# Kernel tuning notes

Measured on AMD Instinct MI355X. Metric: run time of the kernel, lower is better.

The kernel has to match this reference:

```python
import jax, jax.numpy as jnp
import numpy as np

B, L, D, Q, H = 16, 2048, 1024, 1024, 256
NEG_NUM = -10000.0


def setup_inputs() -> dict:
    key = jax.random.key(0)
    ks = jax.random.split(key, 8)
    ctx = jax.random.normal(ks[0], (B, L, D), dtype=jnp.float32)
    query = jax.random.normal(ks[1], (B, Q), dtype=jnp.float32)
    mask = jax.random.randint(ks[2], (B, L), 0, 2, dtype=jnp.int32)
    # lin_in2proj: Linear(D+Q, H)
    lim1 = 1.0 / np.sqrt(D + Q)
    W1 = jax.random.uniform(ks[3], (H, D + Q), jnp.float32, -lim1, lim1)
    b1 = jax.random.uniform(ks[4], (H,), jnp.float32, -lim1, lim1)
    # lin_proj2score: weight_norm(Linear(H, 1)), dim=0 -> g scalar per row
    lim2 = 1.0 / np.sqrt(H)
    v = jax.random.uniform(ks[5], (1, H), jnp.float32, -lim2, lim2)
    g = jnp.linalg.norm(v).reshape(1, 1)  # weight_norm init: g = ||v||
    b2 = jax.random.uniform(ks[6], (1,), jnp.float32, -lim2, lim2)
    return {"ctx": ctx, "query": query, "mask": mask,
            "W1": W1, "b1": b1, "v": v, "g": g, "b2": b2}


def reference(ctx, query, mask, W1, b1, v, g, b2):
    d = ctx.shape[-1]
    # concat([ctx, query_expanded]) @ W1^T == ctx @ W1c^T + query @ W1q^T
    Wc, Wq = W1[:, :d], W1[:, d:]
    hid = jnp.tanh(jnp.einsum('bld,hd->blh', ctx, Wc)
                   + jnp.einsum('bq,hq->bh', query, Wq)[:, None, :]
                   + b1)                                 # (B, L, H)
    w2 = (g * v / jnp.linalg.norm(v))[0]                 # weight-normed row (H,)
    score = jnp.einsum('blh,h->bl', hid, w2) + b2[0]     # (B, L)
    score = jnp.where(mask == 1, NEG_NUM, score)
    p_ctx = jax.nn.softmax(score, axis=-1)               # (B, L)
    expected_ctx = jnp.einsum('bl,bld->bd', p_ctx, ctx)  # (B, D)
    return expected_ctx, p_ctx
```

## Files before the change

kernel.cpp:

```cpp
#include <hip/hip_runtime.h>
#include <hip/hip_bf16.h>

#define BB 16
#define LCTX 2048
#define DDIM 1024
#define QDIM 1024
#define HDIM 256
#define NEGV -10000.0f

typedef __attribute__((ext_vector_type(8))) short short8;
typedef __attribute__((ext_vector_type(4))) float f32x4;

__device__ inline unsigned short f2bf(float x) {
    unsigned int u = __float_as_uint(x);
    unsigned int r = (u + 0x7fffu + ((u >> 16) & 1u)) >> 16;
    return (unsigned short)r;
}

__global__ __launch_bounds__(256) void k_qproj(const float* __restrict__ query,
                                               const float* __restrict__ W1,
                                               const float* __restrict__ b1,
                                               float* __restrict__ qproj) {
    int bid = blockIdx.x;
    int b = bid >> 6;
    int hq = bid & 63;
    int wid = threadIdx.x >> 6, lane = threadIdx.x & 63;
    int h = hq * 4 + wid;
    const float* q = query + b * QDIM;
    const float* w = W1 + (size_t)h * (DDIM + QDIM) + DDIM;
    float s = 0.f;
    #pragma unroll 4
    for (int k = lane; k < QDIM; k += 64) s += q[k] * w[k];
    #pragma unroll
    for (int o = 32; o; o >>= 1) s += __shfl_down(s, o);
    if (lane == 0) qproj[b * HDIM + h] = s + b1[h];
}

__global__ __launch_bounds__(256) void k_prepw(const float* __restrict__ W1,
                                               const float* __restrict__ v,
                                               const float* __restrict__ g,
                                               unsigned short* __restrict__ Wc_sw,
                                               float* __restrict__ w2) {
    int bid = blockIdx.x;
    if (bid < HDIM) {
        int h = bid;
        const float* src = W1 + (size_t)h * (DDIM + QDIM);
        int hx = h & 7;
        for (int d = threadIdx.x; d < DDIM; d += 256) {
            int kt = d >> 6;
            int s  = (d >> 3) & 7;
            int dl = d & 7;
            int dp = (kt << 6) + ((s ^ hx) << 3) + dl;
            Wc_sw[h * DDIM + dp] = f2bf(src[d]);
        }
    } else {
        __shared__ float red[256];
        float vv = (threadIdx.x < HDIM) ? v[threadIdx.x] : 0.f;
        red[threadIdx.x] = vv * vv;
        __syncthreads();
        for (int o = 128; o; o >>= 1) {
            if (threadIdx.x < o) red[threadIdx.x] += red[threadIdx.x + o];
            __syncthreads();
        }
        float nrm = sqrtf(red[0]);
        if (threadIdx.x < HDIM) w2[threadIdx.x] = g[0] * vv / nrm;
    }
}

__global__ __launch_bounds__(256, 3) void k_score(const float* __restrict__ ctx,
                                                  const unsigned short* __restrict__ Wc_sw,
                                                  const float* __restrict__ qproj,
                                                  const float* __restrict__ w2,
                                                  const float* __restrict__ b2,
                                                  const int* __restrict__ mask,
                                                  float* __restrict__ score_out) {
    __shared__ unsigned short At[64 * 64];
    __shared__ unsigned short Wt[256 * 64];
    int tid = threadIdx.x;
    int wid = tid >> 6, lane = tid & 63;
    int hl = lane & 15, lhi = lane >> 4;
    int bid = blockIdx.x;
    int row0 = bid * 64;
    int b = row0 >> 11;

    float qp[4], wv[4];
    #pragma unroll
    for (int ht = 0; ht < 4; ht++) {
        int h = wid * 64 + ht * 16 + hl;
        qp[ht] = qproj[b * HDIM + h];
        wv[ht] = w2[h];
    }

    f32x4 acc[4][4];
    #pragma unroll
    for (int mt = 0; mt < 4; mt++)
        #pragma unroll
        for (int ht = 0; ht < 4; ht++)
            acc[mt][ht] = (f32x4){0.f, 0.f, 0.f, 0.f};

    int srow = tid >> 2;
    int scol = (tid & 3) * 16;
    const float* csrc = ctx + (size_t)(row0 + srow) * DDIM + scol;
    int c0 = (tid & 3) * 2;
    int sx = srow & 7;

    for (int kt = 0; kt < 16; kt++) {
        #pragma unroll
        for (int i = 0; i < 8; i++) {
            int n = i * 256 + tid;
            const unsigned short* gsrc = Wc_sw + (size_t)(n >> 3) * DDIM + kt * 64 + (n & 7) * 8;
            __builtin_amdgcn_global_load_lds(
                (const __attribute__((address_space(1))) unsigned int*)gsrc,
                (__attribute__((address_space(3))) unsigned int*)(Wt + (i * 256 + (tid & ~63)) * 8),
                16, 0, 0);
        }
        const float* cp = csrc + kt * 64;
        float4 cv0 = *(const float4*)(cp + 0);
        float4 cv1 = *(const float4*)(cp + 4);
        float4 cv2 = *(const float4*)(cp + 8);
        float4 cv3 = *(const float4*)(cp + 12);
        short8 p0 = { (short)f2bf(cv0.x), (short)f2bf(cv0.y), (short)f2bf(cv0.z), (short)f2bf(cv0.w),
                      (short)f2bf(cv1.x), (short)f2bf(cv1.y), (short)f2bf(cv1.z), (short)f2bf(cv1.w) };
        short8 p1 = { (short)f2bf(cv2.x), (short)f2bf(cv2.y), (short)f2bf(cv2.z), (short)f2bf(cv2.w),
                      (short)f2bf(cv3.x), (short)f2bf(cv3.y), (short)f2bf(cv3.z), (short)f2bf(cv3.w) };
        *(short8*)(At + srow * 64 + (((c0 + 0) ^ sx) << 3)) = p0;
        *(short8*)(At + srow * 64 + (((c0 + 1) ^ sx) << 3)) = p1;
        __syncthreads();

        #pragma unroll
        for (int ks = 0; ks < 2; ks++) {
            int s = ks * 4 + lhi;
            short8 af[4], bfr[4];
            #pragma unroll
            for (int mt = 0; mt < 4; mt++) {
                int m = mt * 16 + hl;
                af[mt] = *(const short8*)(At + m * 64 + ((s ^ (m & 7)) << 3));
            }
            #pragma unroll
            for (int ht = 0; ht < 4; ht++) {
                int h = wid * 64 + ht * 16 + hl;
                bfr[ht] = *(const short8*)(Wt + h * 64 + ((s ^ (h & 7)) << 3));
            }
            #pragma unroll
            for (int mt = 0; mt < 4; mt++)
                #pragma unroll
                for (int ht = 0; ht < 4; ht++)
                    acc[mt][ht] = __builtin_amdgcn_mfma_f32_16x16x32_bf16(af[mt], bfr[ht], acc[mt][ht], 0, 0, 0);
        }
        __syncthreads();
    }

    float* sb = (float*)At;
    #pragma unroll
    for (int mt = 0; mt < 4; mt++) {
        #pragma unroll
        for (int r = 0; r < 4; r++) {
            float partial = 0.f;
            #pragma unroll
            for (int ht = 0; ht < 4; ht++) {
                float x = acc[mt][ht][r] + qp[ht];
                x = fminf(fmaxf(x, -15.f), 15.f);
                float e = __expf(2.f * x);
                partial += (e - 1.f) / (e + 1.f) * wv[ht];
            }
            #pragma unroll
            for (int o = 1; o < 16; o <<= 1) partial += __shfl_xor(partial, o);
            if (hl == 0) sb[wid * 64 + mt * 16 + lhi * 4 + r] = partial;
        }
    }
    __syncthreads();
    if (tid < 64) {
        float s = sb[tid] + sb[64 + tid] + sb[128 + tid] + sb[192 + tid] + b2[0];
        int grow = row0 + tid;
        int bb = grow >> 11, ll = grow & 2047;
        if (mask[bb * 2048 + ll] == 1) s = NEGV;
        score_out[grow] = s;
    }
}

__global__ __launch_bounds__(256) void k_softmax(float* __restrict__ p) {
    int b = blockIdx.x;
    float* row = p + b * LCTX;
    __shared__ float red[256];
    float vals[8];
    float mx = -1e30f;
    #pragma unroll
    for (int i = 0; i < 8; i++) { vals[i] = row[threadIdx.x + i * 256]; mx = fmaxf(mx, vals[i]); }
    red[threadIdx.x] = mx;
    __syncthreads();
    for (int o = 128; o; o >>= 1) {
        if (threadIdx.x < o) red[threadIdx.x] = fmaxf(red[threadIdx.x], red[threadIdx.x + o]);
        __syncthreads();
    }
    mx = red[0];
    __syncthreads();
    float sum = 0.f;
    #pragma unroll
    for (int i = 0; i < 8; i++) { vals[i] = __expf(vals[i] - mx); sum += vals[i]; }
    red[threadIdx.x] = sum;
    __syncthreads();
    for (int o = 128; o; o >>= 1) {
        if (threadIdx.x < o) red[threadIdx.x] += red[threadIdx.x + o];
        __syncthreads();
    }
    float inv = 1.f / red[0];
    #pragma unroll
    for (int i = 0; i < 8; i++) row[threadIdx.x + i * 256] = vals[i] * inv;
}

__global__ __launch_bounds__(256) void k_expected(const float* __restrict__ ctx,
                                                  const float* __restrict__ p,
                                                  float* __restrict__ part) {
    int b = blockIdx.x, dc = blockIdx.y, ls = blockIdx.z;
    int t = threadIdx.x;
    int dd = (t & 31) * 4;
    int lp = t >> 5;
    const float* base = ctx + (size_t)b * LCTX * DDIM + dc * 128 + dd;
    const float* pr = p + b * LCTX + ls * 256;
    float4 a = {0.f, 0.f, 0.f, 0.f};
    #pragma unroll 4
    for (int k = 0; k < 32; k++) {
        int l = lp + k * 8;
        float w = pr[l];
        float4 c = *(const float4*)(base + (size_t)(ls * 256 + l) * DDIM);
        a.x += w * c.x; a.y += w * c.y; a.z += w * c.z; a.w += w * c.w;
    }
    __shared__ float red[8][128];
    red[lp][dd + 0] = a.x; red[lp][dd + 1] = a.y; red[lp][dd + 2] = a.z; red[lp][dd + 3] = a.w;
    __syncthreads();
    if (t < 128) {
        float s = 0.f;
        #pragma unroll
        for (int i = 0; i < 8; i++) s += red[i][t];
        part[((size_t)ls * 16 + b) * DDIM + dc * 128 + t] = s;
    }
}

__global__ __launch_bounds__(256) void k_finish(const float* __restrict__ part,
                                                float* __restrict__ out) {
    int idx = blockIdx.x * 256 + threadIdx.x;
    float s = 0.f;
    #pragma unroll
    for (int i = 0; i < 8; i++) s += part[i * 16384 + idx];
    out[idx] = s;
}

extern "C" void kernel_launch(void* const* d_in, const int* in_sizes, int n_in,
                              void* d_out, int out_size, void* d_ws, size_t ws_size,
                              hipStream_t stream) {
    const float* ctx   = (const float*)d_in[0];
    const float* query = (const float*)d_in[1];
    const int*   mask  = (const int*)d_in[2];
    const float* W1    = (const float*)d_in[3];
    const float* b1    = (const float*)d_in[4];
    const float* v     = (const float*)d_in[5];
    const float* g     = (const float*)d_in[6];
    const float* b2    = (const float*)d_in[7];
    float* out_exp = (float*)d_out;
    float* out_p   = (float*)d_out + 16384;

    char* ws = (char*)d_ws;
    unsigned short* Wc_sw = (unsigned short*)ws;
    float* qproj = (float*)(ws + 524288);
    float* w2    = (float*)(ws + 540672);
    float* part  = (float*)(ws + 541696);

    k_qproj  <<<dim3(1024),    256, 0, stream>>>(query, W1, b1, qproj);
    k_prepw  <<<dim3(257),     256, 0, stream>>>(W1, v, g, Wc_sw, w2);
    k_score  <<<dim3(512),     256, 0, stream>>>(ctx, Wc_sw, qproj, w2, b2, mask, out_p);
    k_softmax<<<dim3(16),      256, 0, stream>>>(out_p);
    k_expected<<<dim3(16, 8, 8), 256, 0, stream>>>(ctx, out_p, part);
    k_finish <<<dim3(64),      256, 0, stream>>>(part, out_exp);
}
```

Before: 70.48 us.

## Fuse softmax and weighted context sum into score kernel without max subtraction

Merges the qproj and weight-prep kernels into one launch. The score kernel now computes unnormalized exp(score) per row and immediately accumulates exp-weighted ctx rows from the tile it just loaded, writing per-block partial sums. A small normalization kernel sums the partials and divides by the total. This drops the separate softmax, expected and finish kernels and a second pass over ctx. The max subtraction is dropped, which relies on scores being small enough that exp does not overflow, and masked rows become exactly zero instead of exp(-10000 - max).

```diff
diff --git a/kernel.cpp b/kernel.cpp
--- a/kernel.cpp
+++ b/kernel.cpp
@@ -17,33 +17,30 @@
     return (unsigned short)r;
 }
 
-__global__ __launch_bounds__(256) void k_qproj(const float* __restrict__ query,
-                                               const float* __restrict__ W1,
-                                               const float* __restrict__ b1,
-                                               float* __restrict__ qproj) {
+__global__ __launch_bounds__(256) void k_prep(const float* __restrict__ query,
+                                              const float* __restrict__ W1,
+                                              const float* __restrict__ b1,
+                                              const float* __restrict__ v,
+                                              const float* __restrict__ g,
+                                              float* __restrict__ qproj,
+                                              unsigned short* __restrict__ Wc_sw,
+                                              float* __restrict__ w2) {
     int bid = blockIdx.x;
-    int b = bid >> 6;
-    int hq = bid & 63;
-    int wid = threadIdx.x >> 6, lane = threadIdx.x & 63;
-    int h = hq * 4 + wid;
-    const float* q = query + b * QDIM;
-    const float* w = W1 + (size_t)h * (DDIM + QDIM) + DDIM;
-    float s = 0.f;
-    #pragma unroll 4
-    for (int k = lane; k < QDIM; k += 64) s += q[k] * w[k];
-    #pragma unroll
-    for (int o = 32; o; o >>= 1) s += __shfl_down(s, o);
-    if (lane == 0) qproj[b * HDIM + h] = s + b1[h];
-}
-
-__global__ __launch_bounds__(256) void k_prepw(const float* __restrict__ W1,
-                                               const float* __restrict__ v,
-                                               const float* __restrict__ g,
-                                               unsigned short* __restrict__ Wc_sw,
-                                               float* __restrict__ w2) {
-    int bid = blockIdx.x;
-    if (bid < HDIM) {
-        int h = bid;
+    if (bid < 1024) {
+        int b = bid >> 6;
+        int hq = bid & 63;
+        int wid = threadIdx.x >> 6, lane = threadIdx.x & 63;
+        int h = hq * 4 + wid;
+        const float* q = query + b * QDIM;
+        const float* w = W1 + (size_t)h * (DDIM + QDIM) + DDIM;
+        float s = 0.f;
+        #pragma unroll 4
+        for (int k = lane; k < QDIM; k += 64) s += q[k] * w[k];
+        #pragma unroll
+        for (int o = 32; o; o >>= 1) s += __shfl_down(s, o);
+        if (lane == 0) qproj[b * HDIM + h] = s + b1[h];
+    } else if (bid < 1280) {
+        int h = bid - 1024;
         const float* src = W1 + (size_t)h * (DDIM + QDIM);
         int hx = h & 7;
         for (int d = threadIdx.x; d < DDIM; d += 256) {
@@ -73,7 +70,9 @@
                                                   const float* __restrict__ w2,
                                                   const float* __restrict__ b2,
                                                   const int* __restrict__ mask,
-                                                  float* __restrict__ score_out) {
+                                                  float* __restrict__ e_ws,
+                                                  float* __restrict__ esum_ws,
+                                                  float* __restrict__ part) {
     __shared__ unsigned short At[64 * 64];
     __shared__ unsigned short Wt[256 * 64];
     int tid = threadIdx.x;
@@ -150,7 +149,8 @@
         __syncthreads();
     }
 
-    float* sb = (float*)At;
+    float* sb  = (float*)At;
+    float* sbe = sb + 256;
     #pragma unroll
     for (int mt = 0; mt < 4; mt++) {
         #pragma unroll
@@ -169,80 +169,55 @@
         }
     }
     __syncthreads();
+
     if (tid < 64) {
         float s = sb[tid] + sb[64 + tid] + sb[128 + tid] + sb[192 + tid] + b2[0];
         int grow = row0 + tid;
         int bb = grow >> 11, ll = grow & 2047;
-        if (mask[bb * 2048 + ll] == 1) s = NEGV;
-        score_out[grow] = s;
-    }
-}
-
-__global__ __launch_bounds__(256) void k_softmax(float* __restrict__ p) {
-    int b = blockIdx.x;
-    float* row = p + b * LCTX;
-    __shared__ float red[256];
-    float vals[8];
-    float mx = -1e30f;
-    #pragma unroll
-    for (int i = 0; i < 8; i++) { vals[i] = row[threadIdx.x + i * 256]; mx = fmaxf(mx, vals[i]); }
-    red[threadIdx.x] = mx;
+        float e = (mask[bb * 2048 + ll] == 1) ? 0.f : __expf(s);
+        e_ws[grow] = e;
+        sbe[tid] = e;
+        float tot = e;
+        #pragma unroll
+        for (int o = 32; o; o >>= 1) tot += __shfl_down(tot, o);
+        if (tid == 0) esum_ws[bid] = tot;
+    }
     __syncthreads();
-    for (int o = 128; o; o >>= 1) {
-        if (threadIdx.x < o) red[threadIdx.x] = fmaxf(red[threadIdx.x], red[threadIdx.x + o]);
-        __syncthreads();
-    }
-    mx = red[0];
-    __syncthreads();
-    float sum = 0.f;
-    #pragma unroll
-    for (int i = 0; i < 8; i++) { vals[i] = __expf(vals[i] - mx); sum += vals[i]; }
-    red[threadIdx.x] = sum;
-    __syncthreads();
-    for (int o = 128; o; o >>= 1) {
-        if (threadIdx.x < o) red[threadIdx.x] += red[threadIdx.x + o];
-        __syncthreads();
-    }
-    float inv = 1.f / red[0];
-    #pragma unroll
-    for (int i = 0; i < 8; i++) row[threadIdx.x + i * 256] = vals[i] * inv;
-}
-
-__global__ __launch_bounds__(256) void k_expected(const float* __restrict__ ctx,
-                                                  const float* __restrict__ p,
-                                                  float* __restrict__ part) {
-    int b = blockIdx.x, dc = blockIdx.y, ls = blockIdx.z;
-    int t = threadIdx.x;
-    int dd = (t & 31) * 4;
-    int lp = t >> 5;
-    const float* base = ctx + (size_t)b * LCTX * DDIM + dc * 128 + dd;
-    const float* pr = p + b * LCTX + ls * 256;
-    float4 a = {0.f, 0.f, 0.f, 0.f};
-    #pragma unroll 4
-    for (int k = 0; k < 32; k++) {
-        int l = lp + k * 8;
-        float w = pr[l];
-        float4 c = *(const float4*)(base + (size_t)(ls * 256 + l) * DDIM);
-        a.x += w * c.x; a.y += w * c.y; a.z += w * c.z; a.w += w * c.w;
-    }
-    __shared__ float red[8][128];
-    red[lp][dd + 0] = a.x; red[lp][dd + 1] = a.y; red[lp][dd + 2] = a.z; red[lp][dd + 3] = a.w;
-    __syncthreads();
-    if (t < 128) {
+
+    {
+        int d0 = tid * 4;
+        const float* cb = ctx + (size_t)row0 * DDIM + d0;
+        float4 a = {0.f, 0.f, 0.f, 0.f};
+        #pragma unroll 8
+        for (int l = 0; l < 64; l++) {
+            float el = sbe[l];
+            float4 c = *(const float4*)(cb + (size_t)l * DDIM);
+            a.x += el * c.x; a.y += el * c.y; a.z += el * c.z; a.w += el * c.w;
+        }
+        *(float4*)(part + (size_t)bid * DDIM + d0) = a;
+    }
+}
+
+__global__ __launch_bounds__(256) void k_norm(const float* __restrict__ e_ws,
+                                              const float* __restrict__ esum_ws,
+                                              const float* __restrict__ part,
+                                              float* __restrict__ out_exp,
+                                              float* __restrict__ out_p) {
+    int b = blockIdx.x, dc = blockIdx.y;
+    int tid = threadIdx.x;
+    float se = 0.f;
+    #pragma unroll
+    for (int j = 0; j < 32; j++) se += esum_ws[b * 32 + j];
+    float inv = 1.f / se;
+    if (tid < 128) {
+        int d = dc * 128 + tid;
         float s = 0.f;
         #pragma unroll
-        for (int i = 0; i < 8; i++) s += red[i][t];
-        part[((size_t)ls * 16 + b) * DDIM + dc * 128 + t] = s;
-    }
-}
-
-__global__ __launch_bounds__(256) void k_finish(const float* __restrict__ part,
-                                                float* __restrict__ out) {
-    int idx = blockIdx.x * 256 + threadIdx.x;
-    float s = 0.f;
-    #pragma unroll
-    for (int i = 0; i < 8; i++) s += part[i * 16384 + idx];
-    out[idx] = s;
+        for (int j = 0; j < 32; j++) s += part[(size_t)(b * 32 + j) * DDIM + d];
+        out_exp[b * DDIM + d] = s * inv;
+    }
+    int l = dc * 256 + tid;
+    out_p[b * LCTX + l] = e_ws[b * LCTX + l] * inv;
 }
 
 extern "C" void kernel_launch(void* const* d_in, const int* in_sizes, int n_in,
@@ -263,12 +238,11 @@
     unsigned short* Wc_sw = (unsigned short*)ws;
     float* qproj = (float*)(ws + 524288);
     float* w2    = (float*)(ws + 540672);
-    float* part  = (float*)(ws + 541696);
-
-    k_qproj  <<<dim3(1024),    256, 0, stream>>>(query, W1, b1, qproj);
-    k_prepw  <<<dim3(257),     256, 0, stream>>>(W1, v, g, Wc_sw, w2);
-    k_score  <<<dim3(512),     256, 0, stream>>>(ctx, Wc_sw, qproj, w2, b2, mask, out_p);
-    k_softmax<<<dim3(16),      256, 0, stream>>>(out_p);
-    k_expected<<<dim3(16, 8, 8), 256, 0, stream>>>(ctx, out_p, part);
-    k_finish <<<dim3(64),      256, 0, stream>>>(part, out_exp);
-}
+    float* e_ws  = (float*)(ws + 541696);
+    float* esum  = (float*)(ws + 672768);
+    float* part  = (float*)(ws + 674816);
+
+    k_prep <<<dim3(1281),   256, 0, stream>>>(query, W1, b1, v, g, qproj, Wc_sw, w2);
+    k_score<<<dim3(512),    256, 0, stream>>>(ctx, Wc_sw, qproj, w2, b2, mask, e_ws, esum, part);
+    k_norm <<<dim3(16, 8),  256, 0, stream>>>(e_ws, esum, part, out_exp, out_p);
+}
```

Result: faster. 59.15 us (-16.1%).
